# Optimization experiments

Hardware: AMD Instinct MI355X
Metric: run time of the kernel (lower is better)

Reference implementation:

```python
import jax, jax.numpy as jnp
import numpy as np

IMG_WIDTH = 128


def setup_inputs() -> dict:
    key = jax.random.key(0)
    k1, _ = jax.random.split(key)
    B, C, H, W = 16, 1, 128, IMG_WIDTH
    inp = jax.random.normal(k1, (B, C, H, W), dtype=jnp.float32)
    mask = jnp.ones((B, 1, 1, W), dtype=jnp.float32)  # unused by the module's forward, kept for signature fidelity
    return {"input": inp, "mask": mask}


def reference(input, mask):
    # input: (B, C, H, W); only channel 0 is used, matching input[:, :1, ...]
    B, _, H, W = input.shape
    # RFFT module in the repo: ortho-normalized full 2D FFT -> (real, imag) channels
    k = jnp.fft.fft2(input[:, 0], norm="ortho")  # (B, H, W) complex64
    # separated_masks: one-hot per frequency column -> keep only column i in copy i
    col_onehot = jnp.eye(W, dtype=k.dtype)  # (W_copy, W_freq)
    # repeat k-space W times and zero all but one column per copy: (B, W, H, W)
    masked_k = k[:, None, :, :] * col_onehot[None, :, None, :]
    # IFFT module: ortho-normalized 2D IFFT; forward keeps the real part ([:, 0, ...])
    out = jnp.fft.ifft2(masked_k, norm="ortho").real.astype(input.dtype)
    return out  # (B, img_width, H, W)
```

## Files before the change

### kernel.cpp

```cpp
#include <hip/hip_runtime.h>
#include <math.h>


#define WDIM 128
#define BLK 256

__global__ __launch_bounds__(BLK) void kspace_map_kernel(
    const float* __restrict__ in, float* __restrict__ out) {
    const int bh = blockIdx.x;
    const int b  = bh >> 7;
    const int h  = bh & 127;

    __shared__ float x[WDIM];
    __shared__ float cosT[WDIM];
    __shared__ float sinT[WDIM];
    __shared__ float c[WDIM];
    __shared__ float s[WDIM];
    __shared__ float cpart[BLK];
    __shared__ float spart[BLK];

    const int t = threadIdx.x;

    if (t < WDIM) {
        double ang = (double)t * (M_PI / 64.0);
        cosT[t] = (float)cos(ang);
        sinT[t] = (float)sin(ang);
    } else {
        const int w = t - WDIM;
        x[w] = in[(size_t)bh * WDIM + w];
    }
    __syncthreads();

    {
        const int i    = t & 127;
        const int half = t >> 7;
        const int base = half << 6;
        const float stC = cosT[i];
        const float stS = sinT[i];
        float C = (half & i & 1) ? -1.0f : 1.0f;
        float S = 0.0f;
        float cc = 0.0f, ss = 0.0f;
        #pragma unroll
        for (int k = 0; k < 64; ++k) {
            const float xv = x[base + k];
            cc = fmaf(xv, C, cc);
            ss = fmaf(xv, S, ss);
            const float nC = fmaf(C, stC, -(S * stS));
            const float nS = fmaf(S, stC,  (C * stS));
            C = nC; S = nS;
        }
        cpart[t] = cc;
        spart[t] = ss;
    }
    __syncthreads();
    if (t < WDIM) {
        c[t] = cpart[t] + cpart[t + 128];
        s[t] = spart[t] + spart[t + 128];
    }
    __syncthreads();

    const float invW = 1.0f / (float)WDIM;
    const int col   = t & 31;
    const int r     = t >> 5;
    const int wbase = col << 2;
    float* outp = out + ((size_t)b << 21) + ((size_t)h << 7);

    const int qidx = (col << 5) & 127;
    const float qC = cosT[qidx];
    const float qS = sinT[qidx];
    {
        const int idx0 = (r * wbase) & 127;
        float C = cosT[idx0];
        float S = sinT[idx0];

        #pragma unroll
        for (int ii = 0; ii < 16; ++ii) {
            const int i = r + (ii << 3);
            const float ci  = c[i] * invW;
            const float si  = s[i] * invW;
            const float stC = cosT[i];
            const float stS = sinT[i];

            float4 v;
            v.x = fmaf(ci, C, si * S);
            float C1 = fmaf(C, stC, -(S * stS));
            float S1 = fmaf(S, stC,  (C * stS));
            v.y = fmaf(ci, C1, si * S1);
            float C2 = fmaf(C1, stC, -(S1 * stS));
            float S2 = fmaf(S1, stC,  (C1 * stS));
            v.z = fmaf(ci, C2, si * S2);
            float C3 = fmaf(C2, stC, -(S2 * stS));
            float S3 = fmaf(S2, stC,  (C2 * stS));
            v.w = fmaf(ci, C3, si * S3);

            *reinterpret_cast<float4*>(outp + ((size_t)i << 14) + wbase) = v;

            const float nC = fmaf(C, qC, -(S * qS));
            const float nS = fmaf(S, qC,  (C * qS));
            C = nC; S = nS;
        }
    }
}

extern "C" void kernel_launch(void* const* d_in, const int* in_sizes, int n_in,
                              void* d_out, int out_size, void* d_ws, size_t ws_size,
                              hipStream_t stream) {
    const float* in = (const float*)d_in[0];
    float* out = (float*)d_out;
    const int B = 16, H = 128;
    dim3 grid(B * H);
    dim3 block(BLK);
    hipLaunchKernelGGL(kspace_map_kernel, grid, block, 0, stream, in, out);
}
```

Measured before the change: 27.91 us.

## Split each row across four blocks and compute twiddles with fast intrinsics

The grid grows fourfold so that each block handles 32 of the 128 frequency columns for one (b,h) row. The partial DFT is spread over 8 segments of 16 samples and then reduced. The shared cos/sin tables built with double-precision trig are replaced by __cosf/__sinf computed directly in registers. This spreads the large output write (32 MB) over more blocks and removes the slow double trig, at the cost of loading each input row four times and possibly losing some accuracy from the fast intrinsics.

```diff
diff --git a/kernel.cpp b/kernel.cpp
--- a/kernel.cpp
+++ b/kernel.cpp
@@ -4,58 +4,72 @@
 
 #define WDIM 128
 #define BLK 256
+#define PI_OVER_64 0.04908738521234052f
 
 __global__ __launch_bounds__(BLK) void kspace_map_kernel(
     const float* __restrict__ in, float* __restrict__ out) {
-    const int bh = blockIdx.x;
-    const int b  = bh >> 7;
-    const int h  = bh & 127;
+    const int blk = blockIdx.x;
+    const int bh  = blk >> 2;
+    const int q   = blk & 3;
+    const int b   = bh >> 7;
+    const int h   = bh & 127;
 
     __shared__ float x[WDIM];
-    __shared__ float cosT[WDIM];
-    __shared__ float sinT[WDIM];
-    __shared__ float c[WDIM];
-    __shared__ float s[WDIM];
     __shared__ float cpart[BLK];
     __shared__ float spart[BLK];
+    __shared__ float cS[32];
+    __shared__ float sS[32];
 
     const int t = threadIdx.x;
 
-    if (t < WDIM) {
-        double ang = (double)t * (M_PI / 64.0);
-        cosT[t] = (float)cos(ang);
-        sinT[t] = (float)sin(ang);
-    } else {
-        const int w = t - WDIM;
-        x[w] = in[(size_t)bh * WDIM + w];
+    if (t < WDIM) x[t] = in[(size_t)bh * WDIM + t];
+
+    const int il  = t & 31;
+    const int seg = t >> 5;
+    const int ig1 = (q << 5) + il;
+    const int k0  = seg << 4;
+
+    float C, S, stC, stS;
+    {
+        const int idx0 = (ig1 * k0) & 127;
+        const float a0 = (float)idx0 * PI_OVER_64;
+        C = __cosf(a0);
+        S = __sinf(a0);
+        const float as = (float)ig1 * PI_OVER_64;
+        stC = __cosf(as);
+        stS = __sinf(as);
     }
     __syncthreads();
 
     {
-        const int i    = t & 127;
-        const int half = t >> 7;
-        const int base = half << 6;
-        const float stC = cosT[i];
-        const float stS = sinT[i];
-        float C = (half & i & 1) ? -1.0f : 1.0f;
-        float S = 0.0f;
-        float cc = 0.0f, ss = 0.0f;
+        float cc = 0.0f, sc = 0.0f;
         #pragma unroll
-        for (int k = 0; k < 64; ++k) {
-            const float xv = x[base + k];
+        for (int k = 0; k < 16; ++k) {
+            const float xv = x[k0 + k];
             cc = fmaf(xv, C, cc);
-            ss = fmaf(xv, S, ss);
+            sc = fmaf(xv, S, sc);
             const float nC = fmaf(C, stC, -(S * stS));
             const float nS = fmaf(S, stC,  (C * stS));
             C = nC; S = nS;
         }
         cpart[t] = cc;
-        spart[t] = ss;
+        spart[t] = sc;
     }
     __syncthreads();
-    if (t < WDIM) {
-        c[t] = cpart[t] + cpart[t + 128];
-        s[t] = spart[t] + spart[t + 128];
+
+    if (t < 64) {
+        const int j = t & 31;
+        if (t < 32) {
+            float a = 0.f;
+            #pragma unroll
+            for (int g = 0; g < 8; ++g) a += cpart[j + (g << 5)];
+            cS[j] = a;
+        } else {
+            float a = 0.f;
+            #pragma unroll
+            for (int g = 0; g < 8; ++g) a += spart[j + (g << 5)];
+            sS[j] = a;
+        }
     }
     __syncthreads();
 
@@ -65,40 +79,34 @@
     const int wbase = col << 2;
     float* outp = out + ((size_t)b << 21) + ((size_t)h << 7);
 
-    const int qidx = (col << 5) & 127;
-    const float qC = cosT[qidx];
-    const float qS = sinT[qidx];
-    {
-        const int idx0 = (r * wbase) & 127;
-        float C = cosT[idx0];
-        float S = sinT[idx0];
+    #pragma unroll
+    for (int ii = 0; ii < 4; ++ii) {
+        const int ir = r + (ii << 3);
+        const int ig = (q << 5) + ir;
+        const float ci = cS[ir] * invW;
+        const float si = sS[ir] * invW;
 
-        #pragma unroll
-        for (int ii = 0; ii < 16; ++ii) {
-            const int i = r + (ii << 3);
-            const float ci  = c[i] * invW;
-            const float si  = s[i] * invW;
-            const float stC = cosT[i];
-            const float stS = sinT[i];
+        const int idx0 = (ig * wbase) & 127;
+        const float a0 = (float)idx0 * PI_OVER_64;
+        float Cv = __cosf(a0);
+        float Sv = __sinf(a0);
+        const float as = (float)ig * PI_OVER_64;
+        const float rC = __cosf(as);
+        const float rS = __sinf(as);
 
-            float4 v;
-            v.x = fmaf(ci, C, si * S);
-            float C1 = fmaf(C, stC, -(S * stS));
-            float S1 = fmaf(S, stC,  (C * stS));
-            v.y = fmaf(ci, C1, si * S1);
-            float C2 = fmaf(C1, stC, -(S1 * stS));
-            float S2 = fmaf(S1, stC,  (C1 * stS));
-            v.z = fmaf(ci, C2, si * S2);
-            float C3 = fmaf(C2, stC, -(S2 * stS));
-            float S3 = fmaf(S2, stC,  (C2 * stS));
-            v.w = fmaf(ci, C3, si * S3);
+        float4 v;
+        v.x = fmaf(ci, Cv, si * Sv);
+        float C1 = fmaf(Cv, rC, -(Sv * rS));
+        float S1 = fmaf(Sv, rC,  (Cv * rS));
+        v.y = fmaf(ci, C1, si * S1);
+        float C2 = fmaf(C1, rC, -(S1 * rS));
+        float S2 = fmaf(S1, rC,  (C1 * rS));
+        v.z = fmaf(ci, C2, si * S2);
+        float C3 = fmaf(C2, rC, -(S2 * rS));
+        float S3 = fmaf(S2, rC,  (C2 * rS));
+        v.w = fmaf(ci, C3, si * S3);
 
-            *reinterpret_cast<float4*>(outp + ((size_t)i << 14) + wbase) = v;
-
-            const float nC = fmaf(C, qC, -(S * qS));
-            const float nS = fmaf(S, qC,  (C * qS));
-            C = nC; S = nS;
-        }
+        *reinterpret_cast<float4*>(outp + ((size_t)ig << 14) + wbase) = v;
     }
 }
 
@@ -108,7 +116,7 @@
     const float* in = (const float*)d_in[0];
     float* out = (float*)d_out;
     const int B = 16, H = 128;
-    dim3 grid(B * H);
+    dim3 grid(B * H * 4);
     dim3 block(BLK);
     hipLaunchKernelGGL(kspace_map_kernel, grid, block, 0, stream, in, out);
 }
```

Result: faster. 27.00 us, median of 2 (-3.2%).
